# Kernel tuning notes

Hardware: AMD Instinct MI355X
Metric: run time of the kernel (lower is better)

Reference implementation:

```python
import jax, jax.numpy as jnp
import numpy as np


def lut_quantize(v, lut):
    """Nearest-neighbor LUT quantization with straight-through estimator.
    lut is sorted ascending; uses searchsorted (no [N, L] blowup)."""
    L = lut.shape[0]
    idx = jnp.clip(jnp.searchsorted(lut, v), 1, L - 1)
    left = jnp.take(lut, idx - 1)
    right = jnp.take(lut, idx)
    q = jnp.where(v - left <= right - v, left, right)
    return v + jax.lax.stop_gradient(q - v)


def mem_conv(x, w, b, lut):
    # memConv2d: weights/bias snapped to LUT levels, then standard 3x3 SAME conv (NCHW/OIHW)
    wq = lut_quantize(w, lut)
    bq = lut_quantize(b, lut)
    y = jax.lax.conv_general_dilated(x, wq, window_strides=(1, 1),
                                     padding=((1, 1), (1, 1)),
                                     dimension_numbers=('NCHW', 'OIHW', 'NCHW'))
    return y + bq[None, :, None, None]


def mem_linear(x, w, b, lut):
    # memLinear: torch-style weight (out, in)
    return x @ lut_quantize(w, lut).T + lut_quantize(b, lut)


def mem_relu(x, lut):
    # memReLu: ReLU followed by LUT quantization of the activation
    return lut_quantize(jnp.maximum(x, 0.0), lut)


def max_pool_2x2(x):
    return jax.lax.reduce_window(x, -jnp.inf, jax.lax.max,
                                 (1, 1, 2, 2), (1, 1, 2, 2), 'VALID')


def _forward(x, lut, w1, b1, w2, b2, w3, b3, w4, b4, w5, b5, w6, b6,
             fw1, fb1, fw2, fb2, fw3, fb3):
    x = mem_relu(mem_conv(x, w1, b1, lut), lut)
    x = mem_relu(mem_conv(x, w2, b2, lut), lut)
    x = max_pool_2x2(x)                      # [B,32,16,16]
    x = mem_relu(mem_conv(x, w3, b3, lut), lut)
    x = mem_relu(mem_conv(x, w4, b4, lut), lut)
    x = max_pool_2x2(x)                      # [B,64,8,8]
    x = mem_relu(mem_conv(x, w5, b5, lut), lut)
    x = mem_relu(mem_conv(x, w6, b6, lut), lut)
    x = max_pool_2x2(x)                      # [B,128,4,4]
    x = x.reshape(-1, 128 * 4 * 4)
    x = mem_relu(mem_linear(x, fw1, fb1, lut), lut)
    x = mem_relu(mem_linear(x, fw2, fb2, lut), lut)
    x = mem_linear(x, fw3, fb3, lut)
    return jax.nn.softmax(x, axis=1)


def setup_inputs() -> dict:
    key = jax.random.key(0)
    ks = jax.random.split(key, 20)
    B = 512
    lut = jnp.linspace(-4.0, 4.0, 129).astype(jnp.float32)

    def conv_w(k, co, ci):
        scale = np.sqrt(2.0 / (ci * 9)).astype(np.float32)
        return jax.random.normal(k, (co, ci, 3, 3), jnp.float32) * scale

    def lin_w(k, co, ci):
        scale = np.sqrt(2.0 / ci).astype(np.float32)
        return jax.random.normal(k, (co, ci), jnp.float32) * scale

    return {
        'x': jax.random.normal(ks[0], (B, 3, 32, 32), jnp.float32),
        'lut': lut,
        'w1': conv_w(ks[1], 32, 3),   'b1': jnp.zeros((32,), jnp.float32),
        'w2': conv_w(ks[2], 32, 32),  'b2': jnp.zeros((32,), jnp.float32),
        'w3': conv_w(ks[3], 64, 32),  'b3': jnp.zeros((64,), jnp.float32),
        'w4': conv_w(ks[4], 64, 64),  'b4': jnp.zeros((64,), jnp.float32),
        'w5': conv_w(ks[5], 128, 64), 'b5': jnp.zeros((128,), jnp.float32),
        'w6': conv_w(ks[6], 128, 128),'b6': jnp.zeros((128,), jnp.float32),
        'fw1': lin_w(ks[7], 512, 2048), 'fb1': jnp.zeros((512,), jnp.float32),
        'fw2': lin_w(ks[8], 128, 512),  'fb2': jnp.zeros((128,), jnp.float32),
        'fw3': lin_w(ks[9], 10, 128),   'fb3': jnp.zeros((10,), jnp.float32),
    }


def reference(x, lut, w1, b1, w2, b2, w3, b3, w4, b4, w5, b5, w6, b6,
              fw1, fb1, fw2, fb2, fw3, fb3):
    return _forward(x, lut, w1, b1, w2, b2, w3, b3, w4, b4, w5, b5, w6, b6,
                    fw1, fb1, fw2, fb2, fw3, fb3)
```

## Files before the change

kernel.cpp:

```cpp
#include <hip/hip_runtime.h>
#include <cstddef>


#define B_SZ 512
typedef unsigned int u32;
typedef __attribute__((ext_vector_type(4))) int i32x4;

__device__ __forceinline__ float lutq(float v) {
    float k = ceilf(v * 16.0f - 0.5f);
    k = fminf(64.0f, fmaxf(-64.0f, k));
    return k * 0.0625f;
}
__device__ __forceinline__ int kq(float x) {
    float kf = ceilf(x * 16.0f - 0.5f);
    kf = fminf(64.0f, fmaxf(-64.0f, kf));
    return (int)kf;
}
__device__ __forceinline__ u32 bmax4u(u32 a, u32 b) {
    u32 r = 0;
    #pragma unroll
    for (int j = 0; j < 4; ++j) {
        u32 x = (a >> (8 * j)) & 255u, y = (b >> (8 * j)) & 255u;
        r |= (x > y ? x : y) << (8 * j);
    }
    return r;
}

__device__ __forceinline__ void prep_conv_frag(const float* __restrict__ w, char* __restrict__ q,
                                               int i, int CI) {
    int NSTEP = (9 * CI + 63) / 64;
    int e = i & 15, t = i >> 4;
    int ln = t & 63, t2 = t >> 6;
    int s = t2 % NSTEP, co_tile = t2 / NSTEP;
    int k = s * 64 + ((ln >> 4) << 4) + e;
    int tap = k / CI, ci = k % CI;
    int co = co_tile * 16 + (ln & 15);
    int val = 0;
    if (tap < 9) val = kq(w[(co * CI + ci) * 9 + tap]);
    q[i] = (char)val;
}
__device__ __forceinline__ void prep_fc_frag(const float* __restrict__ w, char* __restrict__ q,
                                             int i, int K) {
    int S = K >> 6;
    int e = i & 15, t = i >> 4;
    int ln = t & 63, t2 = t >> 6;
    int s = t2 % S, n_tile = t2 / S;
    int n = n_tile * 16 + (ln & 15);
    int k = s * 64 + ((ln >> 4) << 4) + e;
    q[i] = (char)kq(w[(size_t)n * K + k]);
}

__global__ __launch_bounds__(256) void prep_conv1(
    const float* __restrict__ w2, const float* __restrict__ w3, const float* __restrict__ w4,
    const float* __restrict__ w5, const float* __restrict__ w6,
    const float* __restrict__ fw1, const float* __restrict__ fw2,
    char* q2, char* q3, char* q4, char* q5, char* q6, char* qf1, char* qf2,
    const float* __restrict__ x, const float* __restrict__ w1,
    const float* __restrict__ b1, char* __restrict__ out)
{
    const int tid = threadIdx.x;
    const int bid = blockIdx.x;
    if (bid < 5480) {
        int i = bid * 256 + tid;
        if (i < 10240)                  { prep_conv_frag(w2, q2, i, 32);  }
        else if ((i -= 10240) < 20480)  { prep_conv_frag(w3, q3, i, 32);  }
        else if ((i -= 20480) < 36864)  { prep_conv_frag(w4, q4, i, 64);  }
        else if ((i -= 36864) < 73728)  { prep_conv_frag(w5, q5, i, 64);  }
        else if ((i -= 73728) < 147456) { prep_conv_frag(w6, q6, i, 128); }
        else if ((i -= 147456) < 1048576){ prep_fc_frag(fw1, qf1, i, 2048); }
        else if ((i -= 1048576) < 65536) { prep_fc_frag(fw2, qf2, i, 512);  }
        return;
    }
    __shared__ float s_w[3][9][32];
    __shared__ float s_b[32];
    __shared__ float s_in[3][10][34];
    const int bx  = bid - 5480;
    const int b   = bx >> 2;
    const int r0  = (bx & 3) * 8;
    for (int i = tid; i < 864; i += 256) {
        int o = i % 32, k = (i / 32) % 9, c = i / 288;
        s_w[c][k][o] = lutq(w1[(o * 3 + c) * 9 + k]);
    }
    if (tid < 32) s_b[tid] = lutq(b1[tid]);
    for (int i = tid; i < 3 * 10 * 34; i += 256) {
        int xx = i % 34, yy = (i / 34) % 10, c = i / 340;
        int gy = r0 + yy - 1, gx = xx - 1;
        float v = 0.f;
        if ((unsigned)gy < 32u && (unsigned)gx < 32u)
            v = x[(((size_t)b * 3 + c) * 32 + gy) * 32 + gx];
        s_in[c][yy][xx] = v;
    }
    __syncthreads();
    const int y = tid >> 5, xx = tid & 31;
    float acc[32];
    #pragma unroll
    for (int o = 0; o < 32; ++o) acc[o] = 0.f;
    #pragma unroll
    for (int c = 0; c < 3; ++c) {
        #pragma unroll
        for (int k = 0; k < 9; ++k) {
            float iv = s_in[c][y + k / 3][xx + k % 3];
            #pragma unroll
            for (int o = 0; o < 32; ++o) acc[o] = fmaf(iv, s_w[c][k][o], acc[o]);
        }
    }
    u32 u[8];
    #pragma unroll
    for (int j = 0; j < 8; ++j) {
        u32 p = 0;
        #pragma unroll
        for (int q = 0; q < 4; ++q) {
            float v = fmaxf(acc[4 * j + q] + s_b[4 * j + q], 0.f);
            int kk = (int)ceilf(v * 16.0f - 0.5f);
            kk = kk > 64 ? 64 : kk;
            p |= ((u32)kk & 255u) << (8 * q);
        }
        u[j] = p;
    }
    const int p = (b << 10) + ((r0 + y) << 5) + xx;
    u32* o4 = (u32*)(out + (size_t)p * 32);
    #pragma unroll
    for (int j = 0; j < 8; ++j) o4[j] = u[j];
}

template<int HW, int CI, int CO, int RS, int NIMG, int NT, int POOL = 0>
__global__ __launch_bounds__(256) void conv_mfma(
    const char* __restrict__ in,
    const char* __restrict__ wq,
    const float* __restrict__ bias,
    char* __restrict__ out)
{
    constexpr int PH  = HW + 2;
    constexpr int PIX = NIMG * (RS + 2) * PH;
    constexpr int M   = NIMG * RS * HW;
    constexpr int MT  = M / 16;
    constexpr int MW  = MT / 4;
    constexpr int NSTEP = (9 * CI + 63) / 64;
    constexpr int SL  = HW / RS;
    constexpr int NC16 = CI / 16;
    constexpr int NTC = NT * 16;

    __shared__ __align__(128) char s_in[PIX * CI];

    const int tid = threadIdx.x;
    const int g   = blockIdx.x;
    const int b0  = (g / SL) * NIMG;
    const int r0  = (g % SL) * RS;
    const int co0 = blockIdx.y * NTC;

    constexpr int TOTC = PIX * NC16;
    for (int i = tid; i < TOTC; i += 256) {
        int c16 = i % NC16;
        int pp  = i / NC16;
        int xx  = pp % PH;
        int rr  = pp / PH;
        int yy  = rr % (RS + 2);
        int img = rr / (RS + 2);
        int gy = r0 + yy - 1, gx = xx - 1;
        uint4 v = {0u, 0u, 0u, 0u};
        if ((unsigned)gy < (unsigned)HW && (unsigned)gx < (unsigned)HW)
            v = *(const uint4*)(in + ((((size_t)(b0 + img) * HW + gy) * HW + gx) * CI + c16 * 16));
        int off = (pp * CI + c16 * 16) ^ ((pp & 7) << 4);
        *(uint4*)(s_in + off) = v;
    }
    __syncthreads();

    const int wv = tid >> 6, ln = tid & 63;
    const int l15 = ln & 15, lq = ln >> 4;

    int ppad[MW];
    #pragma unroll
    for (int mw = 0; mw < MW; ++mw) {
        int p = (wv * MW + mw) * 16 + l15;
        int img = p / (RS * HW);
        int rem = p % (RS * HW);
        int ly = rem / HW, lx = rem % HW;
        ppad[mw] = (img * (RS + 2) + ly + 1) * PH + lx + 1;
    }

    i32x4 acc[MW][NT] = {};

    const char* wtile = wq + ((size_t)blockIdx.y * NT) * NSTEP * 1024 + (ln << 4);
    auto dp = [](int t) { return (t / 3 - 1) * PH + (t % 3 - 1); };

    #pragma unroll
    for (int s = 0; s < NSTEP; ++s) {
        i32x4 bf[NT];
        #pragma unroll
        for (int nt = 0; nt < NT; ++nt)
            bf[nt] = *(const i32x4*)(wtile + ((nt * NSTEP + s) << 10));
        int dd, ci0;
        if constexpr (CI == 32) {
            int d0 = dp(2 * s);
            int d1 = (2 * s + 1 < 9) ? dp(2 * s + 1) : 0;
            dd  = (lq & 2) ? d1 : d0;
            ci0 = (lq & 1) << 4;
        } else if constexpr (CI == 64) {
            dd  = dp(s);
            ci0 = lq << 4;
        } else {
            dd  = dp(s >> 1);
            ci0 = ((s & 1) << 6) + (lq << 4);
        }
        #pragma unroll
        for (int mw = 0; mw < MW; ++mw) {
            int pix = ppad[mw] + dd;
            int off = (pix * CI + ci0) ^ ((pix & 7) << 4);
            i32x4 af = *(const i32x4*)(s_in + off);
            #pragma unroll
            for (int nt = 0; nt < NT; ++nt)
                acc[mw][nt] = __builtin_amdgcn_mfma_i32_16x16x64_i8(af, bf[nt], acc[mw][nt], 0, 0, 0);
        }
    }

    if constexpr (POOL == 0) {
        #pragma unroll
        for (int nt = 0; nt < NT; ++nt) {
            int kb16 = 16 * kq(bias[co0 + nt * 16 + l15]);
            #pragma unroll
            for (int mw = 0; mw < MW; ++mw) {
                #pragma unroll
                for (int r = 0; r < 4; ++r) {
                    int p = (wv * MW + mw) * 16 + lq * 4 + r;
                    int img = p / (RS * HW), rem = p % (RS * HW);
                    int ly = rem / HW, lx = rem % HW;
                    int vv = acc[mw][nt][r] + kb16;
                    vv = vv > 0 ? vv : 0;
                    int kk = (vv + 7) >> 4;
                    kk = kk > 64 ? 64 : kk;
                    out[(((size_t)(b0 + img) * HW + r0 + ly) * HW + lx) * CO + co0 + nt * 16 + l15] = (char)kk;
                }
            }
        }
    } else {
        __syncthreads();
        char* s_out = s_in;
        #pragma unroll
        for (int nt = 0; nt < NT; ++nt) {
            int kb16 = 16 * kq(bias[co0 + nt * 16 + l15]);
            #pragma unroll
            for (int mw = 0; mw < MW; ++mw) {
                #pragma unroll
                for (int r = 0; r < 4; ++r) {
                    int p = (wv * MW + mw) * 16 + lq * 4 + r;
                    int vv = acc[mw][nt][r] + kb16;
                    vv = vv > 0 ? vv : 0;
                    int kk = (vv + 7) >> 4;
                    kk = kk > 64 ? 64 : kk;
                    s_out[p * NTC + nt * 16 + l15] = (char)kk;
                }
            }
        }
        __syncthreads();
        constexpr int PR = RS / 2, PC = HW / 2, HOW = HW / 2;
        constexpr int OCT = NIMG * PR * PC * (NTC / 16);
        for (int idx = tid; idx < OCT; idx += 256) {
            int c16 = idx % (NTC / 16);
            int pp  = idx / (NTC / 16);
            int xo = pp % PC, yo = (pp / PC) % PR, img = pp / (PC * PR);
            int pb = (img * RS + 2 * yo) * HW + 2 * xo;
            uint4 v0 = *(const uint4*)(s_out + (pb)          * NTC + c16 * 16);
            uint4 v1 = *(const uint4*)(s_out + (pb + 1)      * NTC + c16 * 16);
            uint4 v2 = *(const uint4*)(s_out + (pb + HW)     * NTC + c16 * 16);
            uint4 v3 = *(const uint4*)(s_out + (pb + HW + 1) * NTC + c16 * 16);
            uint4 r;
            r.x = bmax4u(bmax4u(v0.x, v1.x), bmax4u(v2.x, v3.x));
            r.y = bmax4u(bmax4u(v0.y, v1.y), bmax4u(v2.y, v3.y));
            r.z = bmax4u(bmax4u(v0.z, v1.z), bmax4u(v2.z, v3.z));
            r.w = bmax4u(bmax4u(v0.w, v1.w), bmax4u(v2.w, v3.w));
            if constexpr (POOL == 1) {
                *(uint4*)(out + ((((size_t)(b0 + img) * HOW + (r0 >> 1) + yo) * HOW + xo) * CO
                                 + co0 + c16 * 16)) = r;
            } else {
                const char* rv = (const char*)&r;
                int m = b0 + img;
                #pragma unroll
                for (int j = 0; j < 16; ++j) {
                    int c = co0 + c16 * 16 + j;
                    int k = c * 16 + yo * 4 + xo;
                    int off = (((m >> 4) * 32 + (k >> 6)) << 10)
                            + ((((k >> 4) & 3) * 16 + (m & 15)) << 4) + (k & 15);
                    out[off] = rv[j];
                }
            }
        }
    }
}

__global__ __launch_bounds__(256) void fc1_mfma(
    const char* __restrict__ xa, const char* __restrict__ wq,
    const float* __restrict__ bias, char* __restrict__ out)
{
    constexpr int KS = 2048 / 64;
    const int tid = threadIdx.x, wv = tid >> 6, ln = tid & 63;
    const int l15 = ln & 15, lq = ln >> 4;
    const int m0 = blockIdx.x * 128, n0 = blockIdx.y * 128;
    const int mq = (wv >> 1) * 4, nq = (wv & 1) * 4;
    i32x4 acc[4][4] = {};
    const char* xr[4];
    const char* wt[4];
    #pragma unroll
    for (int t = 0; t < 4; ++t) {
        xr[t] = xa + (size_t)((m0 >> 4) + mq + t) * KS * 1024 + (ln << 4);
        wt[t] = wq + (size_t)((n0 >> 4) + nq + t) * KS * 1024 + (ln << 4);
    }
    #pragma unroll 4
    for (int s = 0; s < KS; ++s) {
        i32x4 a[4], b[4];
        #pragma unroll
        for (int t = 0; t < 4; ++t) {
            a[t] = *(const i32x4*)(xr[t] + (s << 10));
            b[t] = *(const i32x4*)(wt[t] + (s << 10));
        }
        #pragma unroll
        for (int i = 0; i < 4; ++i)
            #pragma unroll
            for (int j = 0; j < 4; ++j)
                acc[i][j] = __builtin_amdgcn_mfma_i32_16x16x64_i8(a[i], b[j], acc[i][j], 0, 0, 0);
    }
    #pragma unroll
    for (int j = 0; j < 4; ++j) {
        int n = n0 + (nq + j) * 16 + l15;
        int kb16 = 16 * kq(bias[n]);
        #pragma unroll
        for (int i = 0; i < 4; ++i)
            #pragma unroll
            for (int r = 0; r < 4; ++r) {
                int m = m0 + (mq + i) * 16 + lq * 4 + r;
                int vv = acc[i][j][r] + kb16;
                vv = vv > 0 ? vv : 0;
                int kk = (vv + 7) >> 4;
                kk = kk > 64 ? 64 : kk;
                out[(size_t)m * 512 + n] = (char)kk;
            }
    }
}

__global__ __launch_bounds__(256) void fc_tail(
    const char* __restrict__ x, const char* __restrict__ qf2,
    const float* __restrict__ fb2, const float* __restrict__ fw3,
    const float* __restrict__ fb3, float* __restrict__ out)
{
    __shared__ __align__(16) char sx[16 * 512];
    __shared__ __align__(16) char sy[16 * 128];
    __shared__ __align__(16) char sw3[10 * 128];
    __shared__ float sb3[10];
    __shared__ int sp[16][16][10];

    const int tid = threadIdx.x;
    const int m0 = blockIdx.x * 16;

    for (int idx = tid; idx < 512; idx += 256) {
        int r = idx >> 5, c16 = idx & 31;
        uint4 v = *(const uint4*)(x + (size_t)(m0 + r) * 512 + c16 * 16);
        *(uint4*)(sx + ((r * 512 + c16 * 16) ^ ((r & 7) << 4))) = v;
    }
    for (int i = tid; i < 1280; i += 256) sw3[i] = (char)kq(fw3[i]);
    if (tid < 10) sb3[tid] = lutq(fb3[tid]);
    __syncthreads();

    const int wv = tid >> 6, ln = tid & 63, l15 = ln & 15, lq = ln >> 4;
    const int ntg = wv * 2;
    i32x4 acc[2] = {};
    #pragma unroll
    for (int s = 0; s < 8; ++s) {
        int row = l15;
        i32x4 a = *(const i32x4*)(sx + ((row * 512 + s * 64 + lq * 16) ^ ((row & 7) << 4)));
        #pragma unroll
        for (int nt = 0; nt < 2; ++nt) {
            i32x4 b = *(const i32x4*)(qf2 + (((ntg + nt) * 8 + s) << 10) + (ln << 4));
            acc[nt] = __builtin_amdgcn_mfma_i32_16x16x64_i8(a, b, acc[nt], 0, 0, 0);
        }
    }
    #pragma unroll
    for (int nt = 0; nt < 2; ++nt) {
        int n = (ntg + nt) * 16 + l15;
        int kb16 = 16 * kq(fb2[n]);
        #pragma unroll
        for (int r = 0; r < 4; ++r) {
            int row = lq * 4 + r;
            int vv = acc[nt][r] + kb16;
            vv = vv > 0 ? vv : 0;
            int kk = (vv + 7) >> 4;
            kk = kk > 64 ? 64 : kk;
            sy[(row * 128 + n) ^ ((row & 7) << 4)] = (char)kk;
        }
    }
    __syncthreads();

    {
        int r = tid >> 4, g = tid & 15;
        uint2 yv = *(const uint2*)(sy + ((r * 128 + g * 8) ^ ((r & 7) << 4)));
        const char* yb = (const char*)&yv;
        #pragma unroll
        for (int o = 0; o < 10; ++o) {
            uint2 wv2 = *(const uint2*)(sw3 + o * 128 + g * 8);
            const char* wb = (const char*)&wv2;
            int S = 0;
            #pragma unroll
            for (int e = 0; e < 8; ++e) S += (int)yb[e] * (int)wb[e];
            sp[r][g][o] = S;
        }
    }
    __syncthreads();

    if (tid < 16) {
        int r = tid;
        float d[10];
        #pragma unroll
        for (int o = 0; o < 10; ++o) {
            int S = 0;
            #pragma unroll
            for (int g = 0; g < 16; ++g) S += sp[r][g][o];
            d[o] = (float)S * 0.00390625f + sb3[o];
        }
        float m = d[0];
        #pragma unroll
        for (int o = 1; o < 10; ++o) m = fmaxf(m, d[o]);
        float e[10];
        float sum = 0.f;
        #pragma unroll
        for (int o = 0; o < 10; ++o) { e[o] = expf(d[o] - m); sum += e[o]; }
        #pragma unroll
        for (int o = 0; o < 10; ++o) out[(size_t)(m0 + r) * 10 + o] = e[o] / sum;
    }
}

extern "C" void kernel_launch(void* const* d_in, const int* in_sizes, int n_in,
                              void* d_out, int out_size, void* d_ws, size_t ws_size,
                              hipStream_t stream)
{
    const float* x   = (const float*)d_in[0];
    const float* w1  = (const float*)d_in[2];
    const float* b1  = (const float*)d_in[3];
    const float* w2  = (const float*)d_in[4];
    const float* b2  = (const float*)d_in[5];
    const float* w3  = (const float*)d_in[6];
    const float* b3  = (const float*)d_in[7];
    const float* w4  = (const float*)d_in[8];
    const float* b4  = (const float*)d_in[9];
    const float* w5  = (const float*)d_in[10];
    const float* b5  = (const float*)d_in[11];
    const float* w6  = (const float*)d_in[12];
    const float* b6  = (const float*)d_in[13];
    const float* fw1 = (const float*)d_in[14];
    const float* fb1 = (const float*)d_in[15];
    const float* fw2 = (const float*)d_in[16];
    const float* fb2 = (const float*)d_in[17];
    const float* fw3 = (const float*)d_in[18];
    const float* fb3 = (const float*)d_in[19];
    float* out = (float*)d_out;

    char* bufA = (char*)d_ws;
    char* bufB = bufA + (16u << 20);
    char* q2  = bufB + (16u << 20);
    char* q3  = q2 + 10240;
    char* q4  = q3 + 20480;
    char* q5  = q4 + 36864;
    char* q6  = q5 + 73728;
    char* qf1 = q6 + 147456;
    char* qf2 = qf1 + 1048576;
    char* fc1out = qf2 + 65536;
    char* fc1a   = fc1out + 262144;

    dim3 blk(256);

    prep_conv1<<<dim3(7528), blk, 0, stream>>>(
        w2, w3, w4, w5, w6, fw1, fw2, q2, q3, q4, q5, q6, qf1, qf2,
        x, w1, b1, bufA);
    conv_mfma<32, 32, 32, 8, 1, 2, 1><<<dim3(2048, 1), blk, 0, stream>>>(bufA, q2, b2, bufB);
    conv_mfma<16, 32, 64, 16, 1, 4, 0><<<dim3(512, 1), blk, 0, stream>>>(bufB, q3, b3, bufA);
    conv_mfma<16, 64, 64, 16, 1, 4, 1><<<dim3(512, 1), blk, 0, stream>>>(bufA, q4, b4, bufB);
    conv_mfma<8, 64, 128, 8, 2, 4, 0><<<dim3(256, 2), blk, 0, stream>>>(bufB, q5, b5, bufA);
    conv_mfma<8, 128, 128, 8, 2, 4, 2><<<dim3(256, 2), blk, 0, stream>>>(bufA, q6, b6, fc1a);
    fc1_mfma<<<dim3(4, 4), blk, 0, stream>>>(fc1a, qf1, fb1, fc1out);
    fc_tail<<<dim3(32), blk, 0, stream>>>(fc1out, qf2, fb2, fw3, fb3, out);
}
```

Measured before the change: 109.6 us.

## Split fc1 int8 MFMA GEMM along K with a separate reduction kernel

The fc1 GEMM previously ran on only 16 workgroups, each looping over the full K of 2048. It now splits K into 16 chunks, so 256 workgroups each write int32 partial sums to a workspace buffer. A new reduce kernel sums the partials, adds the quantized bias, and applies the ReLU/LUT quantization. This trades an extra launch and about 16 MB of partial-sum traffic for much better CU occupancy on the mostly idle GPU.

```diff
diff --git a/kernel.cpp b/kernel.cpp
--- a/kernel.cpp
+++ b/kernel.cpp
@@ -287,14 +287,16 @@
     }
 }
 
-__global__ __launch_bounds__(256) void fc1_mfma(
-    const char* __restrict__ xa, const char* __restrict__ wq,
-    const float* __restrict__ bias, char* __restrict__ out)
-{
-    constexpr int KS = 2048 / 64;
+template<int N, int K, int SK>
+__global__ __launch_bounds__(256) void fc1_splitk(
+    const char* __restrict__ xa, const char* __restrict__ wq, int* __restrict__ part)
+{
+    constexpr int KCH = K / SK;
+    constexpr int KS = K / 64;
     const int tid = threadIdx.x, wv = tid >> 6, ln = tid & 63;
     const int l15 = ln & 15, lq = ln >> 4;
     const int m0 = blockIdx.x * 128, n0 = blockIdx.y * 128;
+    const int kb = blockIdx.z * KCH;
     const int mq = (wv >> 1) * 4, nq = (wv & 1) * 4;
     i32x4 acc[4][4] = {};
     const char* xr[4];
@@ -304,8 +306,8 @@
         xr[t] = xa + (size_t)((m0 >> 4) + mq + t) * KS * 1024 + (ln << 4);
         wt[t] = wq + (size_t)((n0 >> 4) + nq + t) * KS * 1024 + (ln << 4);
     }
-    #pragma unroll 4
-    for (int s = 0; s < KS; ++s) {
+    for (int k0 = 0; k0 < KCH; k0 += 64) {
+        const int s = (kb + k0) >> 6;
         i32x4 a[4], b[4];
         #pragma unroll
         for (int t = 0; t < 4; ++t) {
@@ -318,22 +320,34 @@
             for (int j = 0; j < 4; ++j)
                 acc[i][j] = __builtin_amdgcn_mfma_i32_16x16x64_i8(a[i], b[j], acc[i][j], 0, 0, 0);
     }
+    int* pb = part + (size_t)blockIdx.z * (B_SZ * N);
     #pragma unroll
     for (int j = 0; j < 4; ++j) {
         int n = n0 + (nq + j) * 16 + l15;
-        int kb16 = 16 * kq(bias[n]);
         #pragma unroll
         for (int i = 0; i < 4; ++i)
             #pragma unroll
             for (int r = 0; r < 4; ++r) {
                 int m = m0 + (mq + i) * 16 + lq * 4 + r;
-                int vv = acc[i][j][r] + kb16;
-                vv = vv > 0 ? vv : 0;
-                int kk = (vv + 7) >> 4;
-                kk = kk > 64 ? 64 : kk;
-                out[(size_t)m * 512 + n] = (char)kk;
+                pb[(size_t)m * N + n] = acc[i][j][r];
             }
     }
+}
+
+template<int N, int SK>
+__global__ __launch_bounds__(256) void fc_reduce(
+    const int* __restrict__ part, const float* __restrict__ bias, char* __restrict__ out)
+{
+    int i = blockIdx.x * 256 + threadIdx.x;
+    if (i >= B_SZ * N) return;
+    int s = 0;
+    #pragma unroll
+    for (int k = 0; k < SK; ++k) s += part[(size_t)k * (B_SZ * N) + i];
+    int vv = s + 16 * kq(bias[i % N]);
+    vv = vv > 0 ? vv : 0;
+    int kk = (vv + 7) >> 4;
+    kk = kk > 64 ? 64 : kk;
+    out[i] = (char)kk;
 }
 
 __global__ __launch_bounds__(256) void fc_tail(
@@ -460,7 +474,8 @@
     char* q6  = q5 + 73728;
     char* qf1 = q6 + 147456;
     char* qf2 = qf1 + 1048576;
-    char* fc1out = qf2 + 65536;
+    int*  part = (int*)(qf2 + 65536);
+    char* fc1out = (char*)part + (16u << 20);
     char* fc1a   = fc1out + 262144;
 
     dim3 blk(256);
@@ -473,6 +488,7 @@
     conv_mfma<16, 64, 64, 16, 1, 4, 1><<<dim3(512, 1), blk, 0, stream>>>(bufA, q4, b4, bufB);
     conv_mfma<8, 64, 128, 8, 2, 4, 0><<<dim3(256, 2), blk, 0, stream>>>(bufB, q5, b5, bufA);
     conv_mfma<8, 128, 128, 8, 2, 4, 2><<<dim3(256, 2), blk, 0, stream>>>(bufA, q6, b6, fc1a);
-    fc1_mfma<<<dim3(4, 4), blk, 0, stream>>>(fc1a, qf1, fb1, fc1out);
+    fc1_splitk<512, 2048, 16><<<dim3(4, 4, 16), blk, 0, stream>>>(fc1a, qf1, part);
+    fc_reduce<512, 16><<<dim3(1024), blk, 0, stream>>>(part, fb1, fc1out);
     fc_tail<<<dim3(32), blk, 0, stream>>>(fc1out, qf2, fb2, fw3, fb3, out);
 }
```

Result: faster. 97.78 us (-10.7%).
